# Performance work log

Measured on AMD Instinct MI355X. Metric: run time of the kernel, lower is better.

Reference implementation:

```python
import jax, jax.numpy as jnp
import numpy as np

B, C, H, W = 4, 64, 64, 64
DK, DV = 64, 64


def _conv1x1(x, w, b):
    # x: [B,C,H,W], w: [O,C], b: [O] -> [B,O,H,W]
    return jnp.einsum('bchw,oc->bohw', x, w) + b[None, :, None, None]


def _ordered_mask(N, ordering, dtype):
    mask = jnp.tril(jnp.ones((N, N), dtype=dtype))
    if ordering == 1:
        return mask
    elif ordering == 2:
        return jnp.flip(mask, 1)
    elif ordering == 3:
        return jnp.rot90(mask, 1)
    elif ordering == 4:
        return jnp.flip(jnp.rot90(mask, 1), 0)
    elif ordering == 5:
        return jnp.rot90(mask, 2)
    elif ordering == 6:
        return jnp.flip(jnp.rot90(mask, 2), 1)
    elif ordering == 7:
        return jnp.rot90(mask, 3)
    elif ordering == 8:
        return jnp.flip(jnp.rot90(mask, 3), 1)
    return None


def setup_inputs() -> dict:
    key = jax.random.key(0)
    ks = jax.random.split(key, 9)
    s = 0.02
    return {
        'x': jax.random.normal(ks[0], (B, C, H, W), dtype=jnp.float32),
        'Wq': jax.random.normal(ks[1], (DK, C), dtype=jnp.float32) * s,
        'bq': jnp.zeros((DK,), dtype=jnp.float32),
        'Wk': jax.random.normal(ks[2], (DK, C), dtype=jnp.float32) * s,
        'bk': jnp.zeros((DK,), dtype=jnp.float32),
        'Wv': jax.random.normal(ks[3], (DV, C), dtype=jnp.float32) * s,
        'bv': jnp.zeros((DV,), dtype=jnp.float32),
        'Wo': jax.random.normal(ks[4], (DV, DV + C), dtype=jnp.float32) * s,
        'bo': jnp.zeros((DV,), dtype=jnp.float32),
        'ordering': 1,
    }


def reference(x, Wq, bq, Wk, bk, Wv, bv, Wo, bo, ordering):
    b, c, h, w = x.shape
    N = h * w
    dk, dv = Wq.shape[0], Wv.shape[0]
    Q = _conv1x1(x, Wq, bq).reshape(b, dk, N)  # [B,dk,N]
    K = _conv1x1(x, Wk, bk).reshape(b, dk, N)  # [B,dk,N]
    V = _conv1x1(x, Wv, bv).reshape(b, dv, N)  # [B,dv,N]
    logits = jnp.einsum('bdn,bdm->bnm', Q, K)  # [B,N,N] (no 1/sqrt(dk) scaling, matching source)
    weights = jax.nn.softmax(logits, axis=-1)
    m = _ordered_mask(N, ordering, x.dtype)
    if m is not None:
        weights = weights * m  # post-softmax multiplicative mask
    o = jnp.einsum('bnm,bdm->bdn', weights, V).reshape(b, dv, h, w)
    oc = jnp.concatenate([o, x], axis=1)  # [B,dv+C,H,W]
    return _conv1x1(oc, Wo, bo)
```

## Files before the change

### kernel.cpp

```cpp
#include <hip/hip_runtime.h>

typedef __attribute__((ext_vector_type(8))) short short8;
typedef __attribute__((ext_vector_type(4))) short short4v;
typedef __attribute__((ext_vector_type(4))) float f32x4;
typedef __attribute__((ext_vector_type(16))) float f32x16;
typedef __attribute__((ext_vector_type(4))) unsigned int uint4v;
typedef __attribute__((ext_vector_type(2))) unsigned int uint2v;
typedef unsigned short us;
typedef unsigned int u32;

#define NB 4
#define NC 64
#define NN 4096
#define ND 64
#define LOG2E 1.44269504088896340736f

static __device__ __forceinline__ us f2bf(float x) {
    u32 u = __builtin_bit_cast(u32, x);
    u += 0x7FFFu + ((u >> 16) & 1u);
    return (us)(u >> 16);
}

static __device__ __forceinline__ u32 cvtpk(float a, float b) {
    u32 r;
    asm("v_cvt_pk_bf16_f32 %0, %1, %2" : "=v"(r) : "v"(a), "v"(b));
    return r;
}

static __device__ __forceinline__ short8 comb(short4v a, short4v b) {
    short8 r;
    r[0] = a[0]; r[1] = a[1]; r[2] = a[2]; r[3] = a[3];
    r[4] = b[0]; r[5] = b[1]; r[6] = b[2]; r[7] = b[3];
    return r;
}

static __device__ __forceinline__ void async_copy16(void* lds, const void* g) {
    __builtin_amdgcn_global_load_lds(
        (const __attribute__((address_space(1))) u32*)g,
        (__attribute__((address_space(3))) u32*)lds, 16, 0, 0);
}

__global__ void cvt_wo_kernel(const float* __restrict__ Wo, us* __restrict__ Wob) {
    int i = blockIdx.x * 256 + threadIdx.x;
    if (i < ND * (ND + NC)) Wob[i] = f2bf(Wo[i]);
}

__global__ __launch_bounds__(256) void proj_kernel(
    const float* __restrict__ x,
    const float* __restrict__ Wq, const float* __restrict__ bq,
    const float* __restrict__ Wk, const float* __restrict__ bk,
    const float* __restrict__ Wv, const float* __restrict__ bv,
    us* __restrict__ Qt, us* __restrict__ Kt,
    us* __restrict__ Vm, us* __restrict__ Xbt)
{
    __shared__ float xs[64][64];
    __shared__ __align__(16) us xT[64][64];
    const int t = threadIdx.x;
    const int bid = blockIdx.x;
    const int role = bid & 1;
    const int v = bid >> 1;
    const int b = v >> 6;
    const int n0 = (v & 63) << 6;
    const float* xb = x + (size_t)b * NC * NN + n0;
    #pragma unroll
    for (int i = 0; i < 4; ++i) {
        int s = t + i * 256;
        int c = s >> 4, col = (s & 15) << 2;
        *(f32x4*)&xs[c][col] = *(const f32x4*)&xb[(size_t)c * NN + col];
    }
    __syncthreads();
    {
        int n = t & 63, cg = t >> 6;
        int c0 = cg << 4;
        u32 pk[8];
        #pragma unroll
        for (int j = 0; j < 8; ++j) {
            float a0 = xs[c0 + 2 * j][n], a1 = xs[c0 + 2 * j + 1][n];
            pk[j] = (u32)f2bf(a0) | ((u32)f2bf(a1) << 16);
        }
        int b0 = (cg * 2) ^ (n & 7), b1 = (cg * 2 + 1) ^ (n & 7);
        *(uint4v*)&xT[n][b0 * 8] = (uint4v){pk[0], pk[1], pk[2], pk[3]};
        *(uint4v*)&xT[n][b1 * 8] = (uint4v){pk[4], pk[5], pk[6], pk[7]};
        if (role == 1) {
            us* dst = Xbt + (size_t)(b * NN + n0 + n) * ND + c0;
            *(uint4v*)dst       = (uint4v){pk[0], pk[1], pk[2], pk[3]};
            *(uint4v*)(dst + 8) = (uint4v){pk[4], pk[5], pk[6], pk[7]};
        }
    }
    __syncthreads();
    const int w = t >> 6, l = t & 63, h = l >> 4, ln = l & 15;
    const int row = w * 16 + ln;
    short8 xq0 = *(const short8*)&xT[row][((h ^ (row & 7)) << 3)];
    short8 xq1 = *(const short8*)&xT[row][(((4 + h) ^ (row & 7)) << 3)];

    if (role == 0) {
        #pragma unroll
        for (int p = 0; p < 2; ++p) {
            const float* W = p ? Wk : Wq;
            const float* bias = p ? bk : bq;
            const float sc = p ? 1.0f : LOG2E;
            us* outp = p ? Kt : Qt;
            #pragma unroll
            for (int di = 0; di < 4; ++di) {
                const int d = di * 16 + ln;
                const float* wr = W + d * 64;
                short8 a0, a1;
                f32x4 f0 = *(const f32x4*)(wr + h * 8);
                f32x4 f1 = *(const f32x4*)(wr + h * 8 + 4);
                f32x4 f2 = *(const f32x4*)(wr + 32 + h * 8);
                f32x4 f3 = *(const f32x4*)(wr + 32 + h * 8 + 4);
                #pragma unroll
                for (int j = 0; j < 4; ++j) {
                    a0[j] = (short)f2bf(f0[j] * sc); a0[4 + j] = (short)f2bf(f1[j] * sc);
                    a1[j] = (short)f2bf(f2[j] * sc); a1[4 + j] = (short)f2bf(f3[j] * sc);
                }
                f32x4 acc = *(const f32x4*)(bias + di * 16 + h * 4);
                acc *= sc;
                acc = __builtin_amdgcn_mfma_f32_16x16x32_bf16(a0, xq0, acc, 0, 0, 0);
                acc = __builtin_amdgcn_mfma_f32_16x16x32_bf16(a1, xq1, acc, 0, 0, 0);
                u32 lo = (u32)f2bf(acc[0]) | ((u32)f2bf(acc[1]) << 16);
                u32 hi = (u32)f2bf(acc[2]) | ((u32)f2bf(acc[3]) << 16);
                *(uint2v*)(outp + (size_t)(b * NN + n0 + row) * ND + di * 16 + h * 4) = (uint2v){lo, hi};
            }
        }
    } else {
        #pragma unroll
        for (int di = 0; di < 4; ++di) {
            const int d = di * 16 + ln;
            const float* wr = Wv + d * 64;
            short8 a0, a1;
            f32x4 f0 = *(const f32x4*)(wr + h * 8);
            f32x4 f1 = *(const f32x4*)(wr + h * 8 + 4);
            f32x4 f2 = *(const f32x4*)(wr + 32 + h * 8);
            f32x4 f3 = *(const f32x4*)(wr + 32 + h * 8 + 4);
            #pragma unroll
            for (int j = 0; j < 4; ++j) {
                a0[j] = (short)f2bf(f0[j]); a0[4 + j] = (short)f2bf(f1[j]);
                a1[j] = (short)f2bf(f2[j]); a1[4 + j] = (short)f2bf(f3[j]);
            }
            f32x4 acc = *(const f32x4*)(bv + di * 16 + h * 4);
            acc = __builtin_amdgcn_mfma_f32_16x16x32_bf16(a0, xq0, acc, 0, 0, 0);
            acc = __builtin_amdgcn_mfma_f32_16x16x32_bf16(a1, xq1, acc, 0, 0, 0);
            us* vp = Vm + (size_t)(b * ND + di * 16 + h * 4) * NN + n0 + row;
            vp[0] = f2bf(acc[0]); vp[NN] = f2bf(acc[1]);
            vp[2 * NN] = f2bf(acc[2]); vp[3 * NN] = f2bf(acc[3]);
        }
    }
}

static __device__ __forceinline__ void mask_bounds32(int pt, int n032, int ng,
    int& lo_n, int& hi_n, int& lo_min, int& lo_max, int& hi_min, int& hi_max)
{
    if (pt == 0)      { lo_n = 0;           hi_n = ng;          lo_min = 0;              lo_max = 0;             hi_min = n032;           hi_max = n032 + 31; }
    else if (pt == 1) { lo_n = NN - 1 - ng; hi_n = NN - 1;      lo_min = NN - 32 - n032; lo_max = NN - 1 - n032; hi_min = NN - 1;         hi_max = NN - 1; }
    else if (pt == 2) { lo_n = ng;          hi_n = NN - 1;      lo_min = n032;           lo_max = n032 + 31;     hi_min = NN - 1;         hi_max = NN - 1; }
    else if (pt == 3) { lo_n = 0;           hi_n = NN - 1 - ng; lo_min = 0;              lo_max = 0;             hi_min = NN - 32 - n032; hi_max = NN - 1 - n032; }
    else              { lo_n = 0;           hi_n = NN - 1;      lo_min = 0;              lo_max = 0;             hi_min = NN - 1;         hi_max = NN - 1; }
}

extern __shared__ __align__(16) us lds_us[];
#define KT_(s, bf) (lds_us + ((s) * 2 + (bf)) * 4096)
#define VT_(s, bf) (lds_us + 32768 + ((s) * 2 + (bf)) * 4096)

__global__ __launch_bounds__(512, 2) void attn_kernel(
    const us* __restrict__ Qt, const us* __restrict__ Kt,
    const us* __restrict__ Vm, const us* __restrict__ Xbt,
    const us* __restrict__ Wob, const float* __restrict__ bo,
    const int* __restrict__ ordp, float* __restrict__ out)
{
    const int tid = threadIdx.x;
    const int w = tid >> 6, l = tid & 63;
    const int hi = l >> 5, ln = l & 31;
    const int mh = w >> 1, nh = w & 1;
    const int bid = blockIdx.x;
    const int vid = (bid & 7) * 32 + (bid >> 3);
    const int b = vid >> 6;
    const int n0 = (vid & 63) << 6;
    const int n032 = n0 + nh * 32;
    const int ng = n032 + ln;

    const int ord = ordp[0];
    int pt = 4;
    if (ord == 1) pt = 0;
    else if (ord == 2 || ord == 3) pt = 1;
    else if (ord == 4 || ord == 5 || ord == 8) pt = 2;
    else if (ord == 6 || ord == 7) pt = 3;
    int lo_n, hi_n, lo_min, lo_max, hi_min, hi_max;
    mask_bounds32(pt, n032, ng, lo_n, hi_n, lo_min, lo_max, hi_min, hi_max);

    const us* kb = Kt + (size_t)b * NN * ND;
    const us* vb = Vm + (size_t)b * ND * NN;
    const us* qrow = Qt + (size_t)(b * NN + n032 + ln) * ND;
    short8 qf0 = *(const short8*)(qrow + 0 * 16 + hi * 8);
    short8 qf1 = *(const short8*)(qrow + 1 * 16 + hi * 8);
    short8 qf2 = *(const short8*)(qrow + 2 * 16 + hi * 8);
    short8 qf3 = *(const short8*)(qrow + 3 * 16 + hi * 8);

    f32x16 O0, O1, Z;
    #pragma unroll
    for (int i = 0; i < 16; ++i) { O0[i] = 0.f; O1[i] = 0.f; Z[i] = 0.f; }
    float Lp = 0.f;

    auto stage = [&](int buf, int t) {
        const int m_base = mh * 1024 + t * 64;
        us* dstK = KT_(mh, buf);
        us* dstV = VT_(mh, buf);
        #pragma unroll
        for (int r = 0; r < 8; ++r) {
            const int rl = r * 8 + (l >> 3);
            const int blk = l & 7;
            if (nh == 0) {
                const us* src = kb + (size_t)(m_base + rl) * ND + ((blk ^ (rl & 7)) << 3);
                async_copy16(dstK + r * 8 * 64, src);
            } else {
                const us* src = vb + (size_t)rl * NN + m_base + ((blk ^ (rl & 7)) << 3);
                async_copy16(dstV + r * 8 * 64, src);
            }
        }
    };

    stage(0, 0);
    for (int t = 0; t < 16; ++t) {
        if (t < 15) {
            stage((t + 1) & 1, t + 1);
            asm volatile("s_waitcnt vmcnt(8)" ::: "memory");
        } else {
            asm volatile("s_waitcnt vmcnt(0)" ::: "memory");
        }
        __builtin_amdgcn_s_barrier();
        __builtin_amdgcn_sched_barrier(0);

        const us* KT = KT_(mh, t & 1);
        const us* VT = VT_(mh, t & 1);
        const int m0 = mh * 1024 + t * 64;
        const bool skip = (m0 + 63 < lo_min) || (m0 > hi_max);
        const bool full = (m0 >= lo_max) && (m0 + 63 <= hi_min);

        __builtin_amdgcn_s_setprio(1);
        #pragma unroll
        for (int mss = 0; mss < 2; ++mss) {
            const int row = mss * 32 + ln;
            const int rs = row & 7;
            short8 a0 = *(const short8*)&KT[row * 64 + (((0 + hi) ^ rs) << 3)];
            short8 a1 = *(const short8*)&KT[row * 64 + (((2 + hi) ^ rs) << 3)];
            short8 a2 = *(const short8*)&KT[row * 64 + (((4 + hi) ^ rs) << 3)];
            short8 a3 = *(const short8*)&KT[row * 64 + (((6 + hi) ^ rs) << 3)];
            f32x16 st = __builtin_amdgcn_mfma_f32_32x32x16_bf16(a0, qf0, Z, 0, 0, 0);
            st = __builtin_amdgcn_mfma_f32_32x32x16_bf16(a1, qf1, st, 0, 0, 0);
            st = __builtin_amdgcn_mfma_f32_32x32x16_bf16(a2, qf2, st, 0, 0, 0);
            st = __builtin_amdgcn_mfma_f32_32x32x16_bf16(a3, qf3, st, 0, 0, 0);

            float p[16];
            #pragma unroll
            for (int r = 0; r < 16; ++r) {
                p[r] = __builtin_amdgcn_exp2f(st[r]);
                Lp += p[r];
            }
            if (skip) continue;
            if (!full) {
                #pragma unroll
                for (int r = 0; r < 16; ++r) {
                    const int mg = m0 + mss * 32 + (r & 3) + 8 * (r >> 2) + 4 * hi;
                    if (mg < lo_n || mg > hi_n) p[r] = 0.f;
                }
            }
            #pragma unroll
            for (int c16 = 0; c16 < 2; ++c16) {
                uint4v pw;
                pw[0] = cvtpk(p[c16 * 8 + 0], p[c16 * 8 + 1]);
                pw[1] = cvtpk(p[c16 * 8 + 2], p[c16 * 8 + 3]);
                pw[2] = cvtpk(p[c16 * 8 + 4], p[c16 * 8 + 5]);
                pw[3] = cvtpk(p[c16 * 8 + 6], p[c16 * 8 + 7]);
                short8 pb = __builtin_bit_cast(short8, pw);
                const int blkA = mss * 4 + c16 * 2;
                {
                    const int rv = ln, rvs = rv & 7;
                    short4v va  = *(const short4v*)&VT[rv * 64 + ((blkA ^ rvs) << 3) + hi * 4];
                    short4v vb2 = *(const short4v*)&VT[rv * 64 + (((blkA + 1) ^ rvs) << 3) + hi * 4];
                    O0 = __builtin_amdgcn_mfma_f32_32x32x16_bf16(comb(va, vb2), pb, O0, 0, 0, 0);
                }
                {
                    const int rv = 32 + ln, rvs = rv & 7;
                    short4v va  = *(const short4v*)&VT[rv * 64 + ((blkA ^ rvs) << 3) + hi * 4];
                    short4v vb2 = *(const short4v*)&VT[rv * 64 + (((blkA + 1) ^ rvs) << 3) + hi * 4];
                    O1 = __builtin_amdgcn_mfma_f32_32x32x16_bf16(comb(va, vb2), pb, O1, 0, 0, 0);
                }
            }
        }
        __builtin_amdgcn_s_setprio(0);
        __builtin_amdgcn_sched_barrier(0);
        __builtin_amdgcn_s_barrier();
    }

    float Lw = Lp + __shfl_xor(Lp, 32);

    float* cO = (float*)lds_us;
    float* cL = (float*)(lds_us + 32768);
    if (mh != 0) {
        const int slot = (mh - 1) * 2 + nh;
        float* dsto = cO + slot * 2048 + ln * 64;
        #pragma unroll
        for (int rq = 0; rq < 4; ++rq) {
            f32x4 s0, s1;
            #pragma unroll
            for (int j = 0; j < 4; ++j) { s0[j] = O0[rq * 4 + j]; s1[j] = O1[rq * 4 + j]; }
            *(f32x4*)&dsto[rq * 8 + hi * 4] = s0;
            *(f32x4*)&dsto[32 + rq * 8 + hi * 4] = s1;
        }
        if (hi == 0) cL[slot * 32 + ln] = Lw;
    }
    __syncthreads();
    if (mh != 0) return;

    float gL = Lw;
    #pragma unroll
    for (int i = 0; i < 3; ++i) gL += cL[(i * 2 + nh) * 32 + ln];
    const float rl2 = 1.0f / gL;

    f32x16 On0 = O0, On1 = O1;
    #pragma unroll
    for (int i = 0; i < 3; ++i) {
        const float* s = cO + (i * 2 + nh) * 2048 + ln * 64;
        #pragma unroll
        for (int rq = 0; rq < 4; ++rq) {
            f32x4 a = *(const f32x4*)&s[rq * 8 + hi * 4];
            f32x4 c = *(const f32x4*)&s[32 + rq * 8 + hi * 4];
            #pragma unroll
            for (int j = 0; j < 4; ++j) { On0[rq * 4 + j] += a[j]; On1[rq * 4 + j] += c[j]; }
        }
    }
    #pragma unroll
    for (int i = 0; i < 16; ++i) { On0[i] *= rl2; On1[i] *= rl2; }

    short8 Bf[8];
    {
        uint4v w0, w1, w2, w3;
        w0[0] = cvtpk(On0[0], On0[1]);   w0[1] = cvtpk(On0[2], On0[3]);
        w0[2] = cvtpk(On0[4], On0[5]);   w0[3] = cvtpk(On0[6], On0[7]);
        w1[0] = cvtpk(On0[8], On0[9]);   w1[1] = cvtpk(On0[10], On0[11]);
        w1[2] = cvtpk(On0[12], On0[13]); w1[3] = cvtpk(On0[14], On0[15]);
        w2[0] = cvtpk(On1[0], On1[1]);   w2[1] = cvtpk(On1[2], On1[3]);
        w2[2] = cvtpk(On1[4], On1[5]);   w2[3] = cvtpk(On1[6], On1[7]);
        w3[0] = cvtpk(On1[8], On1[9]);   w3[1] = cvtpk(On1[10], On1[11]);
        w3[2] = cvtpk(On1[12], On1[13]); w3[3] = cvtpk(On1[14], On1[15]);
        Bf[0] = __builtin_bit_cast(short8, w0);
        Bf[1] = __builtin_bit_cast(short8, w1);
        Bf[2] = __builtin_bit_cast(short8, w2);
        Bf[3] = __builtin_bit_cast(short8, w3);
    }
    const us* xrow = Xbt + (size_t)(b * NN + n032 + ln) * ND;
    #pragma unroll
    for (int c4 = 0; c4 < 4; ++c4)
        Bf[4 + c4] = comb(*(const short4v*)(xrow + c4 * 16 + hi * 4),
                          *(const short4v*)(xrow + c4 * 16 + hi * 4 + 8));

    f32x16 acc0, acc1;
    #pragma unroll
    for (int rq = 0; rq < 4; ++rq) {
        f32x4 b0 = *(const f32x4*)&bo[rq * 8 + hi * 4];
        f32x4 b1 = *(const f32x4*)&bo[32 + rq * 8 + hi * 4];
        #pragma unroll
        for (int j = 0; j < 4; ++j) { acc0[rq * 4 + j] = b0[j]; acc1[rq * 4 + j] = b1[j]; }
    }
    const us* wr0 = Wob + (size_t)ln * 128;
    const us* wr1 = Wob + (size_t)(32 + ln) * 128;
    #pragma unroll
    for (int kc = 0; kc < 8; ++kc) {
        short8 wf0 = comb(*(const short4v*)(wr0 + kc * 16 + hi * 4),
                          *(const short4v*)(wr0 + kc * 16 + hi * 4 + 8));
        short8 wf1 = comb(*(const short4v*)(wr1 + kc * 16 + hi * 4),
                          *(const short4v*)(wr1 + kc * 16 + hi * 4 + 8));
        acc0 = __builtin_amdgcn_mfma_f32_32x32x16_bf16(wf0, Bf[kc], acc0, 0, 0, 0);
        acc1 = __builtin_amdgcn_mfma_f32_32x32x16_bf16(wf1, Bf[kc], acc1, 0, 0, 0);
    }
    #pragma unroll
    for (int r = 0; r < 16; ++r) {
        const int od = (r & 3) + 8 * (r >> 2) + 4 * hi;
        out[((size_t)b * 64 + od) * NN + n032 + ln] = acc0[r];
        out[((size_t)b * 64 + 32 + od) * NN + n032 + ln] = acc1[r];
    }
}

extern "C" void kernel_launch(void* const* d_in, const int* in_sizes, int n_in,
                              void* d_out, int out_size, void* d_ws, size_t ws_size,
                              hipStream_t stream) {
    (void)in_sizes; (void)n_in; (void)out_size; (void)ws_size;
    const float* x  = (const float*)d_in[0];
    const float* Wq = (const float*)d_in[1];
    const float* bq = (const float*)d_in[2];
    const float* Wk = (const float*)d_in[3];
    const float* bk = (const float*)d_in[4];
    const float* Wv = (const float*)d_in[5];
    const float* bv = (const float*)d_in[6];
    const float* Wo = (const float*)d_in[7];
    const float* bo = (const float*)d_in[8];
    const int* ord  = (const int*)d_in[9];
    float* out = (float*)d_out;

    us* Qt  = (us*)d_ws;
    us* Kt  = Qt  + (size_t)NB * NN * ND;
    us* Vm  = Kt  + (size_t)NB * NN * ND;
    us* Xbt = Vm  + (size_t)NB * NN * ND;
    us* Wob = Xbt + (size_t)NB * NN * ND;

    hipFuncSetAttribute(reinterpret_cast<const void*>(attn_kernel),
                        hipFuncAttributeMaxDynamicSharedMemorySize, 131072);

    cvt_wo_kernel<<<dim3(32), dim3(256), 0, stream>>>(Wo, Wob);
    proj_kernel<<<dim3(NB * 64 * 2), dim3(256), 0, stream>>>(
        x, Wq, bq, Wk, bk, Wv, bv, Qt, Kt, Vm, Xbt);
    attn_kernel<<<dim3(256), dim3(512), 131072, stream>>>(
        Qt, Kt, Vm, Xbt, Wob, bo, ord, out);
}
```

Measured before the change: 57.19 us.

## Split key range across two blocks and add separate combine kernel

The attention kernel now splits each query tile's key range into two halves handled by separate blocks, doubling the grid to 512 blocks. Each block uses a 32-key tile and half the LDS, which allows 4 blocks per CU. Blocks skip V staging for fully masked tiles. Partial O and L sums go to global workspace, and a new combine kernel reduces them, normalizes, and applies the output projection. The aim is better CU occupancy and load balance, at the cost of an extra kernel launch and global round-trips for the partials.

```diff
diff --git a/kernel.cpp b/kernel.cpp
--- a/kernel.cpp
+++ b/kernel.cpp
@@ -159,23 +159,25 @@
 }
 
 extern __shared__ __align__(16) us lds_us[];
-#define KT_(s, bf) (lds_us + ((s) * 2 + (bf)) * 4096)
-#define VT_(s, bf) (lds_us + 32768 + ((s) * 2 + (bf)) * 4096)
-
-__global__ __launch_bounds__(512, 2) void attn_kernel(
+#define KT_(s, bf) (lds_us + ((s) * 2 + (bf)) * 2048)
+#define VT_(s, bf) (lds_us + 16384 + ((s) * 2 + (bf)) * 2048)
+
+__global__ __launch_bounds__(512, 4) void attn_kernel(
     const us* __restrict__ Qt, const us* __restrict__ Kt,
-    const us* __restrict__ Vm, const us* __restrict__ Xbt,
-    const us* __restrict__ Wob, const float* __restrict__ bo,
-    const int* __restrict__ ordp, float* __restrict__ out)
+    const us* __restrict__ Vm,
+    const int* __restrict__ ordp,
+    float* __restrict__ Op, float* __restrict__ Lb)
 {
     const int tid = threadIdx.x;
     const int w = tid >> 6, l = tid & 63;
     const int hi = l >> 5, ln = l & 31;
-    const int mh = w >> 1, nh = w & 1;
+    const int s = w >> 1, nh = w & 1;
     const int bid = blockIdx.x;
-    const int vid = (bid & 7) * 32 + (bid >> 3);
-    const int b = vid >> 6;
+    const int vid = (bid & 7) * 64 + (bid >> 3);
+    const int b = vid >> 7;
+    const int msb = (vid >> 6) & 1;
     const int n0 = (vid & 63) << 6;
+    const int mbase = msb << 11;
     const int n032 = n0 + nh * 32;
     const int ng = n032 + ln;
 
@@ -188,6 +190,12 @@
     int lo_n, hi_n, lo_min, lo_max, hi_min, hi_max;
     mask_bounds32(pt, n032, ng, lo_n, hi_n, lo_min, lo_max, hi_min, hi_max);
 
+    int vlo = 0, vhi = NN - 1;
+    if (pt == 0)      { vhi = n0 + 63; }
+    else if (pt == 1) { vlo = NN - 64 - n0; }
+    else if (pt == 2) { vlo = n0; }
+    else if (pt == 3) { vhi = NN - 1 - n0; }
+
     const us* kb = Kt + (size_t)b * NN * ND;
     const us* vb = Vm + (size_t)b * ND * NN;
     const us* qrow = Qt + (size_t)(b * NN + n032 + ln) * ND;
@@ -202,19 +210,25 @@
     float Lp = 0.f;
 
     auto stage = [&](int buf, int t) {
-        const int m_base = mh * 1024 + t * 64;
-        us* dstK = KT_(mh, buf);
-        us* dstV = VT_(mh, buf);
-        #pragma unroll
-        for (int r = 0; r < 8; ++r) {
-            const int rl = r * 8 + (l >> 3);
-            const int blk = l & 7;
-            if (nh == 0) {
+        const int m_base = mbase + s * 512 + t * 32;
+        if (nh == 0) {
+            us* dstK = KT_(s, buf);
+            #pragma unroll
+            for (int r = 0; r < 4; ++r) {
+                const int rl = r * 8 + (l >> 3);
+                const int blk = l & 7;
                 const us* src = kb + (size_t)(m_base + rl) * ND + ((blk ^ (rl & 7)) << 3);
                 async_copy16(dstK + r * 8 * 64, src);
-            } else {
-                const us* src = vb + (size_t)rl * NN + m_base + ((blk ^ (rl & 7)) << 3);
-                async_copy16(dstV + r * 8 * 64, src);
+            }
+        } else {
+            if (m_base + 31 < vlo || m_base > vhi) return;
+            us* dstV = VT_(s, buf);
+            #pragma unroll
+            for (int r = 0; r < 4; ++r) {
+                const int rl = r * 16 + (l >> 2);
+                const int blk = l & 3;
+                const us* src = vb + (size_t)rl * NN + m_base + ((blk ^ (rl & 3)) << 3);
+                async_copy16(dstV + r * 16 * 32, src);
             }
         }
     };
@@ -223,67 +237,68 @@
     for (int t = 0; t < 16; ++t) {
         if (t < 15) {
             stage((t + 1) & 1, t + 1);
-            asm volatile("s_waitcnt vmcnt(8)" ::: "memory");
+            asm volatile("s_waitcnt vmcnt(4)" ::: "memory");
         } else {
             asm volatile("s_waitcnt vmcnt(0)" ::: "memory");
         }
         __builtin_amdgcn_s_barrier();
         __builtin_amdgcn_sched_barrier(0);
 
-        const us* KT = KT_(mh, t & 1);
-        const us* VT = VT_(mh, t & 1);
-        const int m0 = mh * 1024 + t * 64;
-        const bool skip = (m0 + 63 < lo_min) || (m0 > hi_max);
-        const bool full = (m0 >= lo_max) && (m0 + 63 <= hi_min);
+        const us* KT = KT_(s, t & 1);
+        const us* VT = VT_(s, t & 1);
+        const int m0 = mbase + s * 512 + t * 32;
+        const bool skip = (m0 + 31 < lo_min) || (m0 > hi_max);
+        const bool full = (m0 >= lo_max) && (m0 + 31 <= hi_min);
 
         __builtin_amdgcn_s_setprio(1);
-        #pragma unroll
-        for (int mss = 0; mss < 2; ++mss) {
-            const int row = mss * 32 + ln;
-            const int rs = row & 7;
-            short8 a0 = *(const short8*)&KT[row * 64 + (((0 + hi) ^ rs) << 3)];
-            short8 a1 = *(const short8*)&KT[row * 64 + (((2 + hi) ^ rs) << 3)];
-            short8 a2 = *(const short8*)&KT[row * 64 + (((4 + hi) ^ rs) << 3)];
-            short8 a3 = *(const short8*)&KT[row * 64 + (((6 + hi) ^ rs) << 3)];
+        {
+            const int rs = ln & 7;
+            short8 a0 = *(const short8*)&KT[ln * 64 + (((0 + hi) ^ rs) << 3)];
+            short8 a1 = *(const short8*)&KT[ln * 64 + (((2 + hi) ^ rs) << 3)];
+            short8 a2 = *(const short8*)&KT[ln * 64 + (((4 + hi) ^ rs) << 3)];
+            short8 a3 = *(const short8*)&KT[ln * 64 + (((6 + hi) ^ rs) << 3)];
             f32x16 st = __builtin_amdgcn_mfma_f32_32x32x16_bf16(a0, qf0, Z, 0, 0, 0);
             st = __builtin_amdgcn_mfma_f32_32x32x16_bf16(a1, qf1, st, 0, 0, 0);
             st = __builtin_amdgcn_mfma_f32_32x32x16_bf16(a2, qf2, st, 0, 0, 0);
             st = __builtin_amdgcn_mfma_f32_32x32x16_bf16(a3, qf3, st, 0, 0, 0);
 
             float p[16];
+            float lp0 = 0.f, lp1 = 0.f;
             #pragma unroll
             for (int r = 0; r < 16; ++r) {
                 p[r] = __builtin_amdgcn_exp2f(st[r]);
-                Lp += p[r];
-            }
-            if (skip) continue;
-            if (!full) {
+                if (r & 1) lp1 += p[r]; else lp0 += p[r];
+            }
+            Lp += lp0 + lp1;
+            if (!skip) {
+                if (!full) {
+                    #pragma unroll
+                    for (int r = 0; r < 16; ++r) {
+                        const int mg = m0 + (r & 3) + 8 * (r >> 2) + 4 * hi;
+                        if (mg < lo_n || mg > hi_n) p[r] = 0.f;
+                    }
+                }
                 #pragma unroll
-                for (int r = 0; r < 16; ++r) {
-                    const int mg = m0 + mss * 32 + (r & 3) + 8 * (r >> 2) + 4 * hi;
-                    if (mg < lo_n || mg > hi_n) p[r] = 0.f;
-                }
-            }
-            #pragma unroll
-            for (int c16 = 0; c16 < 2; ++c16) {
-                uint4v pw;
-                pw[0] = cvtpk(p[c16 * 8 + 0], p[c16 * 8 + 1]);
-                pw[1] = cvtpk(p[c16 * 8 + 2], p[c16 * 8 + 3]);
-                pw[2] = cvtpk(p[c16 * 8 + 4], p[c16 * 8 + 5]);
-                pw[3] = cvtpk(p[c16 * 8 + 6], p[c16 * 8 + 7]);
-                short8 pb = __builtin_bit_cast(short8, pw);
-                const int blkA = mss * 4 + c16 * 2;
-                {
-                    const int rv = ln, rvs = rv & 7;
-                    short4v va  = *(const short4v*)&VT[rv * 64 + ((blkA ^ rvs) << 3) + hi * 4];
-                    short4v vb2 = *(const short4v*)&VT[rv * 64 + (((blkA + 1) ^ rvs) << 3) + hi * 4];
-                    O0 = __builtin_amdgcn_mfma_f32_32x32x16_bf16(comb(va, vb2), pb, O0, 0, 0, 0);
-                }
-                {
-                    const int rv = 32 + ln, rvs = rv & 7;
-                    short4v va  = *(const short4v*)&VT[rv * 64 + ((blkA ^ rvs) << 3) + hi * 4];
-                    short4v vb2 = *(const short4v*)&VT[rv * 64 + (((blkA + 1) ^ rvs) << 3) + hi * 4];
-                    O1 = __builtin_amdgcn_mfma_f32_32x32x16_bf16(comb(va, vb2), pb, O1, 0, 0, 0);
+                for (int c16 = 0; c16 < 2; ++c16) {
+                    uint4v pw;
+                    pw[0] = cvtpk(p[c16 * 8 + 0], p[c16 * 8 + 1]);
+                    pw[1] = cvtpk(p[c16 * 8 + 2], p[c16 * 8 + 3]);
+                    pw[2] = cvtpk(p[c16 * 8 + 4], p[c16 * 8 + 5]);
+                    pw[3] = cvtpk(p[c16 * 8 + 6], p[c16 * 8 + 7]);
+                    short8 pb = __builtin_bit_cast(short8, pw);
+                    const int blkA = c16 * 2;
+                    {
+                        const int rv = ln, rvs = rv & 3;
+                        short4v va  = *(const short4v*)&VT[rv * 32 + ((blkA ^ rvs) << 3) + hi * 4];
+                        short4v vb2 = *(const short4v*)&VT[rv * 32 + (((blkA + 1) ^ rvs) << 3) + hi * 4];
+                        O0 = __builtin_amdgcn_mfma_f32_32x32x16_bf16(comb(va, vb2), pb, O0, 0, 0, 0);
+                    }
+                    {
+                        const int rv = 32 + ln, rvs = rv & 3;
+                        short4v va  = *(const short4v*)&VT[rv * 32 + ((blkA ^ rvs) << 3) + hi * 4];
+                        short4v vb2 = *(const short4v*)&VT[rv * 32 + (((blkA + 1) ^ rvs) << 3) + hi * 4];
+                        O1 = __builtin_amdgcn_mfma_f32_32x32x16_bf16(comb(va, vb2), pb, O1, 0, 0, 0);
+                    }
                 }
             }
         }
@@ -295,9 +310,10 @@
     float Lw = Lp + __shfl_xor(Lp, 32);
 
     float* cO = (float*)lds_us;
-    float* cL = (float*)(lds_us + 32768);
-    if (mh != 0) {
-        const int slot = (mh - 1) * 2 + nh;
+    float* cL = (float*)(lds_us + 49152 * 2 / 2);
+    cL = (float*)((char*)lds_us + 49152);
+    if (s != 0) {
+        const int slot = (s - 1) * 2 + nh;
         float* dsto = cO + slot * 2048 + ln * 64;
         #pragma unroll
         for (int rq = 0; rq < 4; ++rq) {
@@ -310,25 +326,58 @@
         if (hi == 0) cL[slot * 32 + ln] = Lw;
     }
     __syncthreads();
-    if (mh != 0) return;
+    if (s != 0) return;
 
     float gL = Lw;
     #pragma unroll
     for (int i = 0; i < 3; ++i) gL += cL[(i * 2 + nh) * 32 + ln];
+
+    f32x16 On0 = O0, On1 = O1;
+    #pragma unroll
+    for (int i = 0; i < 3; ++i) {
+        const float* sp = cO + (i * 2 + nh) * 2048 + ln * 64;
+        #pragma unroll
+        for (int rq = 0; rq < 4; ++rq) {
+            f32x4 a = *(const f32x4*)&sp[rq * 8 + hi * 4];
+            f32x4 c = *(const f32x4*)&sp[32 + rq * 8 + hi * 4];
+            #pragma unroll
+            for (int j = 0; j < 4; ++j) { On0[rq * 4 + j] += a[j]; On1[rq * 4 + j] += c[j]; }
+        }
+    }
+
+    float* opb = Op + ((size_t)(msb * NB + b) * 64) * NN;
+    #pragma unroll
+    for (int r = 0; r < 16; ++r) {
+        const int d0 = (r & 3) + 8 * (r >> 2) + 4 * hi;
+        opb[(size_t)d0 * NN + n032 + ln] = On0[r];
+        opb[(size_t)(d0 + 32) * NN + n032 + ln] = On1[r];
+    }
+    if (hi == 0) Lb[(size_t)(msb * NB + b) * NN + n032 + ln] = gL;
+}
+
+__global__ __launch_bounds__(256) void combine_kernel(
+    const float* __restrict__ Op, const float* __restrict__ Lb,
+    const us* __restrict__ Xbt, const us* __restrict__ Wob,
+    const float* __restrict__ bo, float* __restrict__ out)
+{
+    const int t = threadIdx.x;
+    const int w = t >> 6, l = t & 63, hi = l >> 5, ln = l & 31;
+    const int gw = blockIdx.x * 4 + w;
+    const int b = gw >> 7;
+    const int n032 = (gw & 127) << 5;
+    const int q = n032 + ln;
+
+    const float* op0 = Op + ((size_t)b * 64) * NN;
+    const float* op1 = Op + ((size_t)(NB + b) * 64) * NN;
+    f32x16 On0, On1;
+    #pragma unroll
+    for (int r = 0; r < 16; ++r) {
+        const int d0 = (r & 3) + 8 * (r >> 2) + 4 * hi;
+        On0[r] = op0[(size_t)d0 * NN + q] + op1[(size_t)d0 * NN + q];
+        On1[r] = op0[(size_t)(d0 + 32) * NN + q] + op1[(size_t)(d0 + 32) * NN + q];
+    }
+    const float gL = Lb[(size_t)b * NN + q] + Lb[(size_t)(NB + b) * NN + q];
     const float rl2 = 1.0f / gL;
-
-    f32x16 On0 = O0, On1 = O1;
-    #pragma unroll
-    for (int i = 0; i < 3; ++i) {
-        const float* s = cO + (i * 2 + nh) * 2048 + ln * 64;
-        #pragma unroll
-        for (int rq = 0; rq < 4; ++rq) {
-            f32x4 a = *(const f32x4*)&s[rq * 8 + hi * 4];
-            f32x4 c = *(const f32x4*)&s[32 + rq * 8 + hi * 4];
-            #pragma unroll
-            for (int j = 0; j < 4; ++j) { On0[rq * 4 + j] += a[j]; On1[rq * 4 + j] += c[j]; }
-        }
-    }
     #pragma unroll
     for (int i = 0; i < 16; ++i) { On0[i] *= rl2; On1[i] *= rl2; }
 
@@ -348,7 +397,7 @@
         Bf[2] = __builtin_bit_cast(short8, w2);
         Bf[3] = __builtin_bit_cast(short8, w3);
     }
-    const us* xrow = Xbt + (size_t)(b * NN + n032 + ln) * ND;
+    const us* xrow = Xbt + (size_t)(b * NN + q) * ND;
     #pragma unroll
     for (int c4 = 0; c4 < 4; ++c4)
         Bf[4 + c4] = comb(*(const short4v*)(xrow + c4 * 16 + hi * 4),
@@ -376,8 +425,8 @@
     #pragma unroll
     for (int r = 0; r < 16; ++r) {
         const int od = (r & 3) + 8 * (r >> 2) + 4 * hi;
-        out[((size_t)b * 64 + od) * NN + n032 + ln] = acc0[r];
-        out[((size_t)b * 64 + 32 + od) * NN + n032 + ln] = acc1[r];
+        out[((size_t)b * 64 + od) * NN + q] = acc0[r];
+        out[((size_t)b * 64 + 32 + od) * NN + q] = acc1[r];
     }
 }
 
@@ -402,13 +451,15 @@
     us* Vm  = Kt  + (size_t)NB * NN * ND;
     us* Xbt = Vm  + (size_t)NB * NN * ND;
     us* Wob = Xbt + (size_t)NB * NN * ND;
+    float* Op = (float*)(Wob + ND * (ND + NC));
+    float* Lb = Op + (size_t)2 * NB * 64 * NN;
 
     hipFuncSetAttribute(reinterpret_cast<const void*>(attn_kernel),
-                        hipFuncAttributeMaxDynamicSharedMemorySize, 131072);
+                        hipFuncAttributeMaxDynamicSharedMemorySize, 65536);
 
     cvt_wo_kernel<<<dim3(32), dim3(256), 0, stream>>>(Wo, Wob);
     proj_kernel<<<dim3(NB * 64 * 2), dim3(256), 0, stream>>>(
         x, Wq, bq, Wk, bk, Wv, bv, Qt, Kt, Vm, Xbt);
-    attn_kernel<<<dim3(256), dim3(512), 131072, stream>>>(
-        Qt, Kt, Vm, Xbt, Wob, bo, ord, out);
-}
+    attn_kernel<<<dim3(512), dim3(512), 65536, stream>>>(Qt, Kt, Vm, ord, Op, Lb);
+    combine_kernel<<<dim3(128), dim3(256), 0, stream>>>(Op, Lb, Xbt, Wob, bo, out);
+}
```

After: 65.05 us. +13.7%, slower.
